# Kernel tuning notes

Hardware: AMD Instinct MI355X
Metric: run time of the kernel (lower is better)

## Reference

```python
import jax, jax.numpy as jnp
import numpy as np

FEATURE_DIM = 256
KEEP = 64  # low-frequency block size kept after the pseudo-DCT


def setup_inputs() -> dict:
    key = jax.random.key(0)
    k_x, k_w, k_b = jax.random.split(key, 3)
    B, C, H, W = 32, 3, 512, 512
    x = jax.random.uniform(k_x, (B, C, H, W), dtype=jnp.float32)
    # nn.Linear(64*64, feature_dim): weight [out, in], bias [out]
    fan_in = KEEP * KEEP
    bound = 1.0 / np.sqrt(fan_in)
    fc_w = jax.random.uniform(k_w, (FEATURE_DIM, fan_in), dtype=jnp.float32, minval=-bound, maxval=bound)
    fc_b = jax.random.uniform(k_b, (FEATURE_DIM,), dtype=jnp.float32, minval=-bound, maxval=bound)
    return {"x": x, "fc_w": fc_w, "fc_b": fc_b}


def reference(x, fc_w, fc_b):
    # grayscale conversion (input has 3 channels)
    x_gray = 0.299 * x[:, 0] + 0.587 * x[:, 1] + 0.114 * x[:, 2]  # [B, H, W]
    # "dct2d": FFT along last dim, then FFT along second-to-last, real part
    X = jnp.fft.fft(jnp.fft.fft(x_gray, axis=-1), axis=-2).real  # [B, H, W]
    # keep low-frequency 64x64 block and flatten
    coeffs = X[:, :KEEP, :KEEP].reshape(x.shape[0], KEEP * KEEP)  # [B, 4096]
    # final linear projection
    return coeffs @ fc_w.T + fc_b  # [B, feature_dim]
```

## Files before the change

### kernel.cpp

```cpp
#include <hip/hip_runtime.h>
#include <hip/hip_bf16.h>

#define B_    32
#define H_    512
#define W_    512
#define KEEP_ 64
#define FD_   256
#define FANIN 4096

typedef __attribute__((ext_vector_type(8))) _Float16 half8;
typedef __attribute__((ext_vector_type(4))) float    f32x4;

__global__ __launch_bounds__(256) void k_prep(const float* __restrict__ fc_w,
                                              _Float16* __restrict__ basisA,
                                              _Float16* __restrict__ basisW,
                                              _Float16* __restrict__ fcwb)
{
    int gid    = blockIdx.x * blockDim.x + threadIdx.x;
    int stride = gridDim.x * blockDim.x;
    const float STEP = 6.28318530717958647692f / 512.0f;

    for (int i = gid; i < 128 * 512; i += stride) {
        int r = i >> 9, h = i & 511;
        int ph = ((r & 63) * h) & 511;
        float ang = (float)ph * STEP;
        float v = (r < 64) ? cosf(ang) : sinf(ang);
        basisA[i] = (_Float16)v;
    }
    for (int i = gid; i < 64 * 1024; i += stride) {
        int n = i >> 10, j = i & 1023;
        int ph = (n * (j & 511)) & 511;
        float ang = (float)ph * STEP;
        float v = (j < 512) ? cosf(ang) : -sinf(ang);
        basisW[i] = (_Float16)(v * 0.0625f);
    }
    for (int i = gid; i < 256 * 4096; i += stride)
        fcwb[i] = (_Float16)(fc_w[i] * 16.0f);
}

__global__ __launch_bounds__(256) void k_gray(const float* __restrict__ x,
                                              _Float16* __restrict__ grayT)
{
    int b  = blockIdx.z;
    int h0 = blockIdx.y * 64;
    int w0 = blockIdx.x * 64;
    __shared__ float tile[64][65];

    const float* xb = x + (size_t)b * 3 * H_ * W_;
    int t = threadIdx.x;

    for (int i = 0; i < 4; ++i) {
        int slot = t + i * 256;
        int hh = slot >> 4;
        int w4 = slot & 15;
        const float* p0 = xb + (size_t)(h0 + hh) * W_ + w0 + w4 * 4;
        const float* p1 = p0 + (size_t)H_ * W_;
        const float* p2 = p1 + (size_t)H_ * W_;
        float4 r = *(const float4*)p0;
        float4 g = *(const float4*)p1;
        float4 bl = *(const float4*)p2;
        tile[hh][w4 * 4 + 0] = 0.299f * r.x + 0.587f * g.x + 0.114f * bl.x;
        tile[hh][w4 * 4 + 1] = 0.299f * r.y + 0.587f * g.y + 0.114f * bl.y;
        tile[hh][w4 * 4 + 2] = 0.299f * r.z + 0.587f * g.z + 0.114f * bl.z;
        tile[hh][w4 * 4 + 3] = 0.299f * r.w + 0.587f * g.w + 0.114f * bl.w;
    }
    __syncthreads();

    _Float16* gb = grayT + (size_t)b * W_ * H_;
    for (int i = 0; i < 16; ++i) {
        int idx = t + i * 256;
        int ww = idx >> 6;
        int hh = idx & 63;
        gb[(size_t)(w0 + ww) * H_ + h0 + hh] = (_Float16)tile[hh][ww];
    }
}

__global__ __launch_bounds__(256) void k_stage1(const _Float16* __restrict__ basisA,
                                                const _Float16* __restrict__ grayT,
                                                _Float16* __restrict__ T)
{
    int b  = blockIdx.y;
    int n0 = blockIdx.x * 64;
    int lane = threadIdx.x & 63;
    int wv   = threadIdx.x >> 6;
    int l15  = lane & 15;
    int quad = lane >> 4;

    f32x4 acc[2][4];
    for (int i = 0; i < 2; ++i)
        for (int j = 0; j < 4; ++j)
            acc[i][j] = (f32x4){0.f, 0.f, 0.f, 0.f};

    const _Float16* gb = grayT + (size_t)b * W_ * H_;

    for (int k0 = 0; k0 < 512; k0 += 32) {
        int kc = k0 + quad * 8;
        half8 a[2], bv[4];
        for (int mi = 0; mi < 2; ++mi) {
            int row = wv * 32 + mi * 16 + l15;
            a[mi] = *(const half8*)(basisA + row * 512 + kc);
        }
        for (int ni = 0; ni < 4; ++ni) {
            int row = n0 + ni * 16 + l15;
            bv[ni] = *(const half8*)(gb + (size_t)row * 512 + kc);
        }
        for (int mi = 0; mi < 2; ++mi)
            for (int ni = 0; ni < 4; ++ni)
                acc[mi][ni] = __builtin_amdgcn_mfma_f32_16x16x32_f16(
                    a[mi], bv[ni], acc[mi][ni], 0, 0, 0);
    }

    _Float16* Tb = T + (size_t)b * 64 * 1024;
    for (int mi = 0; mi < 2; ++mi)
        for (int ni = 0; ni < 4; ++ni)
            for (int r = 0; r < 4; ++r) {
                int m = wv * 32 + mi * 16 + quad * 4 + r;
                int n = n0 + ni * 16 + l15;
                int off = (m < 64) ? (m * 1024 + n) : ((m - 64) * 1024 + 512 + n);
                Tb[off] = (_Float16)acc[mi][ni][r];
            }
}

__global__ __launch_bounds__(256) void k_stage2(const _Float16* __restrict__ T,
                                                const _Float16* __restrict__ basisW,
                                                _Float16* __restrict__ X)
{
    int b    = blockIdx.x;
    int lane = threadIdx.x & 63;
    int wv   = threadIdx.x >> 6;
    int l15  = lane & 15;
    int quad = lane >> 4;

    f32x4 acc[4];
    for (int i = 0; i < 4; ++i) acc[i] = (f32x4){0.f, 0.f, 0.f, 0.f};

    const _Float16* Tb = T + (size_t)b * 64 * 1024;

    for (int k0 = 0; k0 < 1024; k0 += 32) {
        int kc = k0 + quad * 8;
        half8 a = *(const half8*)(Tb + (wv * 16 + l15) * 1024 + kc);
        for (int ni = 0; ni < 4; ++ni) {
            half8 bv = *(const half8*)(basisW + (ni * 16 + l15) * 1024 + kc);
            acc[ni] = __builtin_amdgcn_mfma_f32_16x16x32_f16(a, bv, acc[ni], 0, 0, 0);
        }
    }

    _Float16* Xb = X + (size_t)b * 4096;
    for (int ni = 0; ni < 4; ++ni)
        for (int r = 0; r < 4; ++r) {
            int kh = wv * 16 + quad * 4 + r;
            int kw = ni * 16 + l15;
            Xb[kh * 64 + kw] = (_Float16)acc[ni][r];
        }
}

__global__ __launch_bounds__(64) void k_fc(const _Float16* __restrict__ X,
                                           const _Float16* __restrict__ fcwb,
                                           const float* __restrict__ fc_b,
                                           float* __restrict__ out)
{
    int nb   = blockIdx.x & 15;
    int kc   = blockIdx.x >> 4;
    int lane = threadIdx.x;
    int l15  = lane & 15;
    int quad = lane >> 4;

    f32x4 acc[2];
    acc[0] = (f32x4){0.f, 0.f, 0.f, 0.f};
    acc[1] = (f32x4){0.f, 0.f, 0.f, 0.f};

    int kbeg = kc * 1024;
    for (int k0 = kbeg; k0 < kbeg + 1024; k0 += 32) {
        int kk = k0 + quad * 8;
        half8 a0 = *(const half8*)(X + (size_t)(l15)      * 4096 + kk);
        half8 a1 = *(const half8*)(X + (size_t)(16 + l15) * 4096 + kk);
        half8 b0 = *(const half8*)(fcwb + (size_t)(nb * 16 + l15) * 4096 + kk);
        acc[0] = __builtin_amdgcn_mfma_f32_16x16x32_f16(a0, b0, acc[0], 0, 0, 0);
        acc[1] = __builtin_amdgcn_mfma_f32_16x16x32_f16(a1, b0, acc[1], 0, 0, 0);
    }

    for (int mi = 0; mi < 2; ++mi)
        for (int r = 0; r < 4; ++r) {
            int m = mi * 16 + quad * 4 + r;
            int f = nb * 16 + l15;
            float v = acc[mi][r];
            if (kc == 0) v += fc_b[f];
            atomicAdd(out + m * 256 + f, v);
        }
}

extern "C" void kernel_launch(void* const* d_in, const int* in_sizes, int n_in,
                              void* d_out, int out_size, void* d_ws, size_t ws_size,
                              hipStream_t stream) {
    const float* x    = (const float*)d_in[0];
    const float* fc_w = (const float*)d_in[1];
    const float* fc_b = (const float*)d_in[2];
    float* out = (float*)d_out;

    char* ws = (char*)d_ws;
    _Float16* basisA = (_Float16*)(ws + 0);
    _Float16* basisW = (_Float16*)(ws + 131072);
    _Float16* fcwb   = (_Float16*)(ws + 262144);
    _Float16* grayT  = (_Float16*)(ws + 2359296);
    _Float16* T      = (_Float16*)(ws + 19136512);
    _Float16* X      = (_Float16*)(ws + 23330816);

    k_prep<<<512, 256, 0, stream>>>(fc_w, basisA, basisW, fcwb);
    k_gray<<<dim3(8, 8, 32), 256, 0, stream>>>(x, grayT);
    k_stage1<<<dim3(8, 32), 256, 0, stream>>>(basisA, grayT, T);
    k_stage2<<<32, 256, 0, stream>>>(T, basisW, X);
    hipMemsetAsync(d_out, 0, (size_t)out_size * sizeof(float), stream);
    k_fc<<<64, 64, 0, stream>>>(X, fcwb, fc_b, out);
}
```

Measured before the change: 202.5 us.

## Fuse grayscale into row-DFT stage, drop transposed gray buffer and extra basis tables

Grayscale conversion now happens inside the first DFT kernel: each block loads a 32-row strip into shared memory as fp16 and multiplies it by the cosine/sine basis. This removes the 16 MB transposed gray round trip through global memory. The second stage reorders the contraction so it reuses the same basis table, with the sign flip and scale folded in, and it uses more blocks than before. The fc weights are converted to fp16 on the fly inside the final GEMM instead of in the prep kernel. In exchange, the fc weights are read as fp32 (twice the bytes), and the prep kernel now does less work.

```diff
diff --git a/kernel.cpp b/kernel.cpp
--- a/kernel.cpp
+++ b/kernel.cpp
@@ -1,146 +1,99 @@
 #include <hip/hip_runtime.h>
 #include <hip/hip_bf16.h>
 
-#define B_    32
-#define H_    512
-#define W_    512
-#define KEEP_ 64
-#define FD_   256
-#define FANIN 4096
+#define HW_ (512 * 512)
 
 typedef __attribute__((ext_vector_type(8))) _Float16 half8;
+typedef __attribute__((ext_vector_type(4))) _Float16 half4;
 typedef __attribute__((ext_vector_type(4))) float    f32x4;
 
-__global__ __launch_bounds__(256) void k_prep(const float* __restrict__ fc_w,
-                                              _Float16* __restrict__ basisA,
-                                              _Float16* __restrict__ basisW,
-                                              _Float16* __restrict__ fcwb)
-{
-    int gid    = blockIdx.x * blockDim.x + threadIdx.x;
-    int stride = gridDim.x * blockDim.x;
-    const float STEP = 6.28318530717958647692f / 512.0f;
-
-    for (int i = gid; i < 128 * 512; i += stride) {
+__global__ __launch_bounds__(256) void k_prep(_Float16* __restrict__ basisA) {
+    int i = blockIdx.x * 256 + threadIdx.x;
+    if (i < 128 * 512) {
         int r = i >> 9, h = i & 511;
         int ph = ((r & 63) * h) & 511;
-        float ang = (float)ph * STEP;
-        float v = (r < 64) ? cosf(ang) : sinf(ang);
-        basisA[i] = (_Float16)v;
+        float ang = (float)ph * (6.28318530717958647692f / 512.0f);
+        basisA[i] = (_Float16)((r < 64) ? cosf(ang) : sinf(ang));
     }
-    for (int i = gid; i < 64 * 1024; i += stride) {
-        int n = i >> 10, j = i & 1023;
-        int ph = (n * (j & 511)) & 511;
-        float ang = (float)ph * STEP;
-        float v = (j < 512) ? cosf(ang) : -sinf(ang);
-        basisW[i] = (_Float16)(v * 0.0625f);
-    }
-    for (int i = gid; i < 256 * 4096; i += stride)
-        fcwb[i] = (_Float16)(fc_w[i] * 16.0f);
 }
 
-__global__ __launch_bounds__(256) void k_gray(const float* __restrict__ x,
-                                              _Float16* __restrict__ grayT)
+__global__ __launch_bounds__(256) void k1(const float* __restrict__ x,
+                                          const _Float16* __restrict__ basisA,
+                                          _Float16* __restrict__ P)
 {
-    int b  = blockIdx.z;
-    int h0 = blockIdx.y * 64;
-    int w0 = blockIdx.x * 64;
-    __shared__ float tile[64][65];
+    __shared__ _Float16 g[32][520];
+    int h0 = blockIdx.x * 32;
+    int b  = blockIdx.y;
+    int t  = threadIdx.x;
+    const float* xb = x + (size_t)b * 3 * HW_;
 
-    const float* xb = x + (size_t)b * 3 * H_ * W_;
-    int t = threadIdx.x;
-
-    for (int i = 0; i < 4; ++i) {
+    for (int i = 0; i < 16; ++i) {
         int slot = t + i * 256;
-        int hh = slot >> 4;
-        int w4 = slot & 15;
-        const float* p0 = xb + (size_t)(h0 + hh) * W_ + w0 + w4 * 4;
-        const float* p1 = p0 + (size_t)H_ * W_;
-        const float* p2 = p1 + (size_t)H_ * W_;
-        float4 r = *(const float4*)p0;
-        float4 g = *(const float4*)p1;
-        float4 bl = *(const float4*)p2;
-        tile[hh][w4 * 4 + 0] = 0.299f * r.x + 0.587f * g.x + 0.114f * bl.x;
-        tile[hh][w4 * 4 + 1] = 0.299f * r.y + 0.587f * g.y + 0.114f * bl.y;
-        tile[hh][w4 * 4 + 2] = 0.299f * r.z + 0.587f * g.z + 0.114f * bl.z;
-        tile[hh][w4 * 4 + 3] = 0.299f * r.w + 0.587f * g.w + 0.114f * bl.w;
+        int hh = slot >> 7;
+        int w4 = slot & 127;
+        const float* p = xb + (size_t)(h0 + hh) * 512 + w4 * 4;
+        float4 r  = *(const float4*)p;
+        float4 gg = *(const float4*)(p + HW_);
+        float4 bb = *(const float4*)(p + 2 * HW_);
+        half4 o;
+        o.x = (_Float16)(0.299f * r.x + 0.587f * gg.x + 0.114f * bb.x);
+        o.y = (_Float16)(0.299f * r.y + 0.587f * gg.y + 0.114f * bb.y);
+        o.z = (_Float16)(0.299f * r.z + 0.587f * gg.z + 0.114f * bb.z);
+        o.w = (_Float16)(0.299f * r.w + 0.587f * gg.w + 0.114f * bb.w);
+        *(half4*)&g[hh][w4 * 4] = o;
     }
     __syncthreads();
 
-    _Float16* gb = grayT + (size_t)b * W_ * H_;
-    for (int i = 0; i < 16; ++i) {
-        int idx = t + i * 256;
-        int ww = idx >> 6;
-        int hh = idx & 63;
-        gb[(size_t)(w0 + ww) * H_ + h0 + hh] = (_Float16)tile[hh][ww];
-    }
-}
-
-__global__ __launch_bounds__(256) void k_stage1(const _Float16* __restrict__ basisA,
-                                                const _Float16* __restrict__ grayT,
-                                                _Float16* __restrict__ T)
-{
-    int b  = blockIdx.y;
-    int n0 = blockIdx.x * 64;
-    int lane = threadIdx.x & 63;
-    int wv   = threadIdx.x >> 6;
-    int l15  = lane & 15;
-    int quad = lane >> 4;
-
-    f32x4 acc[2][4];
+    int lane = t & 63, wv = t >> 6, l15 = lane & 15, quad = lane >> 4;
+    f32x4 acc[2][2];
     for (int i = 0; i < 2; ++i)
-        for (int j = 0; j < 4; ++j)
-            acc[i][j] = (f32x4){0.f, 0.f, 0.f, 0.f};
-
-    const _Float16* gb = grayT + (size_t)b * W_ * H_;
+        for (int j = 0; j < 2; ++j) acc[i][j] = (f32x4){0.f, 0.f, 0.f, 0.f};
 
     for (int k0 = 0; k0 < 512; k0 += 32) {
         int kc = k0 + quad * 8;
-        half8 a[2], bv[4];
-        for (int mi = 0; mi < 2; ++mi) {
-            int row = wv * 32 + mi * 16 + l15;
-            a[mi] = *(const half8*)(basisA + row * 512 + kc);
-        }
-        for (int ni = 0; ni < 4; ++ni) {
-            int row = n0 + ni * 16 + l15;
-            bv[ni] = *(const half8*)(gb + (size_t)row * 512 + kc);
-        }
+        half8 a[2], bv[2];
         for (int mi = 0; mi < 2; ++mi)
-            for (int ni = 0; ni < 4; ++ni)
+            a[mi] = *(const half8*)(basisA + (wv * 32 + mi * 16 + l15) * 512 + kc);
+        for (int ni = 0; ni < 2; ++ni)
+            bv[ni] = *(const half8*)&g[ni * 16 + l15][kc];
+        for (int mi = 0; mi < 2; ++mi)
+            for (int ni = 0; ni < 2; ++ni)
                 acc[mi][ni] = __builtin_amdgcn_mfma_f32_16x16x32_f16(
                     a[mi], bv[ni], acc[mi][ni], 0, 0, 0);
     }
 
-    _Float16* Tb = T + (size_t)b * 64 * 1024;
+    _Float16* Pb = P + (size_t)b * 128 * 512;
     for (int mi = 0; mi < 2; ++mi)
-        for (int ni = 0; ni < 4; ++ni)
+        for (int ni = 0; ni < 2; ++ni)
             for (int r = 0; r < 4; ++r) {
                 int m = wv * 32 + mi * 16 + quad * 4 + r;
-                int n = n0 + ni * 16 + l15;
-                int off = (m < 64) ? (m * 1024 + n) : ((m - 64) * 1024 + 512 + n);
-                Tb[off] = (_Float16)acc[mi][ni][r];
+                int h = h0 + ni * 16 + l15;
+                float v = acc[mi][ni][r];
+                if (m >= 64) v = -v;
+                Pb[m * 512 + h] = (_Float16)v;
             }
 }
 
-__global__ __launch_bounds__(256) void k_stage2(const _Float16* __restrict__ T,
-                                                const _Float16* __restrict__ basisW,
-                                                _Float16* __restrict__ X)
+__global__ __launch_bounds__(128) void k2(const _Float16* __restrict__ basisA,
+                                          const _Float16* __restrict__ P,
+                                          _Float16* __restrict__ X)
 {
-    int b    = blockIdx.x;
-    int lane = threadIdx.x & 63;
-    int wv   = threadIdx.x >> 6;
-    int l15  = lane & 15;
-    int quad = lane >> 4;
+    int b     = blockIdx.y;
+    int mbase = blockIdx.x * 32 + (threadIdx.x >> 6) * 16;
+    int lane  = threadIdx.x & 63, l15 = lane & 15, quad = lane >> 4;
 
     f32x4 acc[4];
     for (int i = 0; i < 4; ++i) acc[i] = (f32x4){0.f, 0.f, 0.f, 0.f};
 
-    const _Float16* Tb = T + (size_t)b * 64 * 1024;
+    const _Float16* Pb = P + (size_t)b * 128 * 512;
 
     for (int k0 = 0; k0 < 1024; k0 += 32) {
-        int kc = k0 + quad * 8;
-        half8 a = *(const half8*)(Tb + (wv * 16 + l15) * 1024 + kc);
+        int kc  = k0 + quad * 8;
+        int hi  = (kc >= 512) ? 64 : 0;
+        int col = kc & 511;
+        half8 a = *(const half8*)(basisA + (hi + mbase + l15) * 512 + col);
         for (int ni = 0; ni < 4; ++ni) {
-            half8 bv = *(const half8*)(basisW + (ni * 16 + l15) * 1024 + kc);
+            half8 bv = *(const half8*)(Pb + (hi + ni * 16 + l15) * 512 + col);
             acc[ni] = __builtin_amdgcn_mfma_f32_16x16x32_f16(a, bv, acc[ni], 0, 0, 0);
         }
     }
@@ -148,33 +101,42 @@
     _Float16* Xb = X + (size_t)b * 4096;
     for (int ni = 0; ni < 4; ++ni)
         for (int r = 0; r < 4; ++r) {
-            int kh = wv * 16 + quad * 4 + r;
+            int kh = mbase + quad * 4 + r;
             int kw = ni * 16 + l15;
-            Xb[kh * 64 + kw] = (_Float16)acc[ni][r];
+            Xb[kh * 64 + kw] = (_Float16)(acc[ni][r] * 0.0625f);
         }
 }
 
-__global__ __launch_bounds__(64) void k_fc(const _Float16* __restrict__ X,
-                                           const _Float16* __restrict__ fcwb,
-                                           const float* __restrict__ fc_b,
-                                           float* __restrict__ out)
+__global__ __launch_bounds__(64) void k3(const _Float16* __restrict__ X,
+                                         const float* __restrict__ fc_w,
+                                         const float* __restrict__ fc_b,
+                                         float* __restrict__ out)
 {
-    int nb   = blockIdx.x & 15;
-    int kc   = blockIdx.x >> 4;
-    int lane = threadIdx.x;
-    int l15  = lane & 15;
-    int quad = lane >> 4;
+    int nb  = blockIdx.x & 15;
+    int kcb = blockIdx.x >> 4;
+    int lane = threadIdx.x, l15 = lane & 15, quad = lane >> 4;
 
     f32x4 acc[2];
     acc[0] = (f32x4){0.f, 0.f, 0.f, 0.f};
     acc[1] = (f32x4){0.f, 0.f, 0.f, 0.f};
 
-    int kbeg = kc * 1024;
+    int kbeg = kcb * 1024;
     for (int k0 = kbeg; k0 < kbeg + 1024; k0 += 32) {
         int kk = k0 + quad * 8;
-        half8 a0 = *(const half8*)(X + (size_t)(l15)      * 4096 + kk);
+        half8 a0 = *(const half8*)(X + (size_t)l15 * 4096 + kk);
         half8 a1 = *(const half8*)(X + (size_t)(16 + l15) * 4096 + kk);
-        half8 b0 = *(const half8*)(fcwb + (size_t)(nb * 16 + l15) * 4096 + kk);
+        const float* wp = fc_w + (size_t)(nb * 16 + l15) * 4096 + kk;
+        float4 f0 = *(const float4*)wp;
+        float4 f1 = *(const float4*)(wp + 4);
+        half8 b0;
+        b0[0] = (_Float16)(f0.x * 16.0f);
+        b0[1] = (_Float16)(f0.y * 16.0f);
+        b0[2] = (_Float16)(f0.z * 16.0f);
+        b0[3] = (_Float16)(f0.w * 16.0f);
+        b0[4] = (_Float16)(f1.x * 16.0f);
+        b0[5] = (_Float16)(f1.y * 16.0f);
+        b0[6] = (_Float16)(f1.z * 16.0f);
+        b0[7] = (_Float16)(f1.w * 16.0f);
         acc[0] = __builtin_amdgcn_mfma_f32_16x16x32_f16(a0, b0, acc[0], 0, 0, 0);
         acc[1] = __builtin_amdgcn_mfma_f32_16x16x32_f16(a1, b0, acc[1], 0, 0, 0);
     }
@@ -184,7 +146,7 @@
             int m = mi * 16 + quad * 4 + r;
             int f = nb * 16 + l15;
             float v = acc[mi][r];
-            if (kc == 0) v += fc_b[f];
+            if (kcb == 0) v += fc_b[f];
             atomicAdd(out + m * 256 + f, v);
         }
 }
@@ -199,16 +161,12 @@
 
     char* ws = (char*)d_ws;
     _Float16* basisA = (_Float16*)(ws + 0);
-    _Float16* basisW = (_Float16*)(ws + 131072);
-    _Float16* fcwb   = (_Float16*)(ws + 262144);
-    _Float16* grayT  = (_Float16*)(ws + 2359296);
-    _Float16* T      = (_Float16*)(ws + 19136512);
-    _Float16* X      = (_Float16*)(ws + 23330816);
+    _Float16* P      = (_Float16*)(ws + 131072);
+    _Float16* X      = (_Float16*)(ws + 4325376);
 
-    k_prep<<<512, 256, 0, stream>>>(fc_w, basisA, basisW, fcwb);
-    k_gray<<<dim3(8, 8, 32), 256, 0, stream>>>(x, grayT);
-    k_stage1<<<dim3(8, 32), 256, 0, stream>>>(basisA, grayT, T);
-    k_stage2<<<32, 256, 0, stream>>>(T, basisW, X);
+    k_prep<<<256, 256, 0, stream>>>(basisA);
+    k1<<<dim3(16, 32), 256, 0, stream>>>(x, basisA, P);
+    k2<<<dim3(2, 32), 128, 0, stream>>>(basisA, P, X);
     hipMemsetAsync(d_out, 0, (size_t)out_size * sizeof(float), stream);
-    k_fc<<<64, 64, 0, stream>>>(X, fcwb, fc_b, out);
+    k3<<<64, 64, 0, stream>>>(X, fc_w, fc_b, out);
 }
```

New measurement: 188.8 us. 6.8% less time.
